# Kernel optimization log

Hardware: AMD Instinct MI355X
Metric: run time of the kernel (lower is better)

The kernel has to match this reference:

```python
import jax, jax.numpy as jnp
import numpy as np

NUM_HEADS = 12

def setup_inputs() -> dict:
    key = jax.random.key(0)
    ks = jax.random.split(key, 6)
    B, N, C, P = 16, 785, 768, 48
    return {
        "x": jax.random.normal(ks[0], (B, N, C), jnp.float32),
        "qkv_w": jax.random.normal(ks[1], (3 * C, C), jnp.float32) * 0.02,
        "pos_emb": jax.random.normal(ks[2], (N, N, P), jnp.float32) * 0.02,
        "pos_proj_w": jax.random.normal(ks[3], (NUM_HEADS, P), jnp.float32) * 0.02,
        "proj_w": jax.random.normal(ks[4], (C, C), jnp.float32) * 0.02,
        "proj_b": jnp.zeros((C,), jnp.float32),
    }

def reference(x, qkv_w, pos_emb, pos_proj_w, proj_w, proj_b):
    B, N, C = x.shape
    H = NUM_HEADS
    hd = C // H
    scale = hd ** -0.5
    # qkv projection: [B,N,3C] -> q,k,v each [B,H,N,hd]
    qkv = (x @ qkv_w.T).reshape(B, N, 3, H, hd)
    qkv = jnp.transpose(qkv, (2, 0, 3, 1, 4))
    q, k, v = qkv[0], qkv[1], qkv[2]
    # learned relative-position bias: [H,N,N]
    pos_score = jnp.einsum('nmp,hp->hnm', pos_emb, pos_proj_w)
    # attention scores: scale applied AFTER adding bias (matches original)
    attn = (jnp.einsum('bhnd,bhmd->bhnm', q, k) + pos_score[None]) * scale
    attn = jax.nn.softmax(attn, axis=-1)
    out = jnp.einsum('bhnm,bhmd->bhnd', attn, v)
    out = jnp.transpose(out, (0, 2, 1, 3)).reshape(B, N, C)
    return out @ proj_w.T + proj_b
```

## Files before the change

kernel.cpp:

```cpp
#include <hip/hip_runtime.h>
#include <hip/hip_fp16.h>

#define B_ 16
#define N_ 785
#define NP 800
#define C_ 768
#define H_ 12
#define HD_ 64
#define P_ 48
#define M_ (B_*N_)
#define MP_ (B_*NP)
#define POSW 832
#define VTW  832
#define SLOG2E 0.1803368801111244f

#define OFF_Q   0
#define OFF_K   9646080
#define OFF_VT  19292160
#define OFF_POS 29515776
#define OFF_XF  37353216
#define OFF_AO  OFF_XF
#define OFF_WQ  47085312
#define OFF_WP  48854784

struct __align__(16) Half8 { __half h[8]; };
typedef _Float16 half8_t __attribute__((ext_vector_type(8)));
typedef _Float16 half4_t __attribute__((ext_vector_type(4)));
typedef float f32x4 __attribute__((ext_vector_type(4)));

__device__ __forceinline__ void gl16(const void* g, void* l) {
    __builtin_amdgcn_global_load_lds(
        (const __attribute__((address_space(1))) void*)g,
        (__attribute__((address_space(3))) void*)l, 16, 0, 0);
}

__device__ __forceinline__ int xcd_swz(int o, int nwg) {
    const int q = nwg >> 3, r = nwg & 7;
    const int xcd = o & 7, idx = o >> 3;
    const int base = xcd < r ? xcd * (q + 1) : r * (q + 1) + (xcd - r) * q;
    return base + idx;
}

#define NX4 2411520
#define NQ4 442368
#define NP4 147456
#define NTOT4 (NX4+NQ4+NP4)

__global__ __launch_bounds__(256) void convert_f16(
    const float* __restrict__ x, const float* __restrict__ wq,
    const float* __restrict__ wp, _Float16* __restrict__ xo,
    _Float16* __restrict__ wqo, _Float16* __restrict__ wpo)
{
    int i = blockIdx.x * 256 + threadIdx.x;
    const float4* s; _Float16* d; int o;
    if (i < NX4)            { s = (const float4*)x;  d = xo;  o = i; }
    else if (i < NX4 + NQ4) { s = (const float4*)wq; d = wqo; o = i - NX4; }
    else                    { s = (const float4*)wp; d = wpo; o = i - NX4 - NQ4; }
    float4 v = s[o];
    half4_t h = { (_Float16)v.x, (_Float16)v.y, (_Float16)v.z, (_Float16)v.w };
    *(half4_t*)&d[o * 4] = h;
}

#define QKV_NWG (18 * 100)

__global__ __launch_bounds__(256) void qkv_gemm_mfma(
    const _Float16* __restrict__ A, const _Float16* __restrict__ Bw,
    _Float16* __restrict__ qh, _Float16* __restrict__ kh, _Float16* __restrict__ vth)
{
    __shared__ _Float16 Asl[2][128 * 64];
    __shared__ _Float16 Bsl[2][128 * 64];

    const int t  = threadIdx.x;
    const int w  = t >> 6;
    const int l  = t & 63;
    const int lr = l & 15;
    const int lg = l >> 4;
    const int wm = (w >> 1) * 64;
    const int wn = (w & 1) * 64;

    const int g   = xcd_swz(blockIdx.x, QKV_NWG);
    const int nt  = g % 18;
    const int n0  = nt * 128;
    const int mp0 = (g / 18) * 128;
    const int tsel  = nt / 6;
    const bool isV  = (tsel == 2);
    const int nbase = n0 - tsel * 768;

    const int row0 = t >> 2, row1 = 64 + (t >> 2);
    const int within = (t & 3) * 8;
    const int mpa0 = mp0 + row0, mpa1 = mp0 + row1;
    const int xra0 = (mpa0 / NP) * N_ + min(mpa0 % NP, N_ - 1);
    const int xra1 = (mpa1 / NP) * N_ + min(mpa1 % NP, N_ - 1);
    const _Float16* Ag0 = A  + (size_t)xra0 * 768 + within;
    const _Float16* Ag1 = A  + (size_t)xra1 * 768 + within;
    const _Float16* Bg0 = Bw + (size_t)(n0 + row0) * 768 + within;
    const _Float16* Bg1 = Bw + (size_t)(n0 + row1) * 768 + within;
    const int d0 = t * 8, d1 = (t + 256) * 8, d2 = (t + 512) * 8, d3 = (t + 768) * 8;

    f32x4 acc[4][4];
    #pragma unroll
    for (int i = 0; i < 4; ++i)
        #pragma unroll
        for (int j = 0; j < 4; ++j) acc[i][j] = (f32x4){0.f, 0.f, 0.f, 0.f};

    gl16(Ag0, &Asl[0][d0]); gl16(Ag1, &Asl[0][d1]);
    gl16(Ag0 + 32, &Asl[0][d2]); gl16(Ag1 + 32, &Asl[0][d3]);
    gl16(Bg0, &Bsl[0][d0]); gl16(Bg1, &Bsl[0][d1]);
    gl16(Bg0 + 32, &Bsl[0][d2]); gl16(Bg1 + 32, &Bsl[0][d3]);
    __syncthreads();

    for (int it = 0; it < 12; ++it) {
        const int cur = it & 1;
        if (it < 11) {
            const int kn = (it + 1) * 64;
            gl16(Ag0 + kn, &Asl[cur ^ 1][d0]); gl16(Ag1 + kn, &Asl[cur ^ 1][d1]);
            gl16(Ag0 + kn + 32, &Asl[cur ^ 1][d2]); gl16(Ag1 + kn + 32, &Asl[cur ^ 1][d3]);
            gl16(Bg0 + kn, &Bsl[cur ^ 1][d0]); gl16(Bg1 + kn, &Bsl[cur ^ 1][d1]);
            gl16(Bg0 + kn + 32, &Bsl[cur ^ 1][d2]); gl16(Bg1 + kn + 32, &Bsl[cur ^ 1][d3]);
        }
        #pragma unroll
        for (int kk = 0; kk < 2; ++kk) {
            const int kb = kk * 4096;
            half8_t af[4], bf[4];
            #pragma unroll
            for (int i = 0; i < 4; ++i)
                af[i] = *(const half8_t*)&Asl[cur][kb + (wm + i * 16 + lr) * 32 + lg * 8];
            #pragma unroll
            for (int j = 0; j < 4; ++j)
                bf[j] = *(const half8_t*)&Bsl[cur][kb + (wn + j * 16 + lr) * 32 + lg * 8];
            __builtin_amdgcn_s_setprio(1);
            if (!isV) {
                #pragma unroll
                for (int i = 0; i < 4; ++i)
                    #pragma unroll
                    for (int j = 0; j < 4; ++j)
                        acc[i][j] = __builtin_amdgcn_mfma_f32_16x16x32_f16(bf[j], af[i], acc[i][j], 0, 0, 0);
            } else {
                #pragma unroll
                for (int i = 0; i < 4; ++i)
                    #pragma unroll
                    for (int j = 0; j < 4; ++j)
                        acc[i][j] = __builtin_amdgcn_mfma_f32_16x16x32_f16(af[i], bf[j], acc[i][j], 0, 0, 0);
            }
            __builtin_amdgcn_s_setprio(0);
        }
        __syncthreads();
    }

    if (!isV) {
        _Float16* dstb = (tsel == 0) ? qh : kh;
        const float sc  = (tsel == 0) ? SLOG2E : 1.0f;
        #pragma unroll
        for (int i = 0; i < 4; ++i) {
            const int mp = mp0 + wm + i * 16 + lr;
            const int bb = mp / NP;
            const int nn = mp - bb * NP;
            if (nn >= N_) continue;
            #pragma unroll
            for (int j = 0; j < 4; ++j) {
                const int nq = nbase + wn + j * 16 + lg * 4;
                const int hh = nq >> 6, dd = nq & 63;
                half4_t hv = { (_Float16)(acc[i][j][0] * sc), (_Float16)(acc[i][j][1] * sc),
                               (_Float16)(acc[i][j][2] * sc), (_Float16)(acc[i][j][3] * sc) };
                *(half4_t*)(dstb + ((size_t)(bb * H_ + hh) * N_ + nn) * HD_ + dd) = hv;
            }
        }
    } else {
        #pragma unroll
        for (int i = 0; i < 4; ++i) {
            const int mq  = mp0 + wm + i * 16 + lg * 4;
            const int bb  = mq / NP;
            const int nn0 = mq - bb * NP;
            if (nn0 >= N_) continue;
            const bool full = (nn0 + 3) < N_;
            #pragma unroll
            for (int j = 0; j < 4; ++j) {
                const int n  = nbase + wn + j * 16 + lr;
                const int hh = n >> 6, dd = n & 63;
                _Float16* vb = vth + ((size_t)(bb * H_ + hh) * HD_ + dd) * VTW;
                if (full) {
                    half4_t hv = { (_Float16)acc[i][j][0], (_Float16)acc[i][j][1],
                                   (_Float16)acc[i][j][2], (_Float16)acc[i][j][3] };
                    *(half4_t*)(vb + nn0) = hv;
                } else {
                    #pragma unroll
                    for (int r = 0; r < 4; ++r)
                        if (nn0 + r < N_) vb[nn0 + r] = (_Float16)acc[i][j][r];
                }
            }
        }
    }
}

__global__ __launch_bounds__(256) void pos_kernel(
    const float* __restrict__ pe, const float* __restrict__ pw,
    __half* __restrict__ posh)
{
    __shared__ float W[H_][P_];
    const int t = threadIdx.x;
    for (int i = t; i < H_ * P_; i += 256) W[i / P_][i % P_] = pw[i];
    __syncthreads();
    int nm = blockIdx.x * 256 + t;
    if (nm >= N_ * N_) return;
    float e[48];
    const float4* src = (const float4*)(pe + (size_t)nm * 48);
    #pragma unroll
    for (int i = 0; i < 12; ++i) {
        float4 v = src[i];
        e[4*i] = v.x; e[4*i+1] = v.y; e[4*i+2] = v.z; e[4*i+3] = v.w;
    }
    int n = nm / N_, m = nm - n * N_;
    #pragma unroll
    for (int hh = 0; hh < H_; ++hh) {
        float s = 0.f;
        #pragma unroll
        for (int p = 0; p < 48; ++p) s = fmaf(e[p], W[hh][p], s);
        posh[((size_t)hh * N_ + n) * POSW + m] = __float2half(s * SLOG2E);
    }
}

#define NQT 13
#define ATT_NWG (192 * NQT)

__global__ __launch_bounds__(256) void attn_mfma(
    const _Float16* __restrict__ qh, const _Float16* __restrict__ kh,
    const _Float16* __restrict__ vt, const _Float16* __restrict__ posh,
    _Float16* __restrict__ aoh)
{
    __shared__ _Float16 Kl[2][64][72];
    __shared__ _Float16 Vl[2][64][72];

    const int t  = threadIdx.x;
    const int l  = t & 63;
    const int w  = t >> 6;
    const int lr = l & 15;
    const int lg = l >> 4;

    const int g2   = xcd_swz(blockIdx.x, ATT_NWG);
    const int qt   = g2 % NQT;
    const int rest = g2 / NQT;
    const int b    = rest & 15;
    const int h    = rest >> 4;
    const int bh   = b * H_ + h;
    const int n0   = qt * 64;

    const int qrow = n0 + w * 16 + lr;
    const int qrc  = qrow < N_ ? qrow : N_ - 1;
    const _Float16* qbase = qh + ((size_t)bh * N_ + qrc) * HD_;
    const half8_t qf0 = *(const half8_t*)(qbase + lg * 8);
    const half8_t qf1 = *(const half8_t*)(qbase + 32 + lg * 8);

    f32x4 O0 = {0.f,0.f,0.f,0.f}, O1 = O0, O2 = O0, O3 = O0;
    f32x4 lacc = {0.f,0.f,0.f,0.f};
    float m_run = 0.f;
    bool  virgin = true;

    const half8_t vones = { (_Float16)1.f, (_Float16)1.f, (_Float16)1.f, (_Float16)1.f,
                            (_Float16)1.f, (_Float16)1.f, (_Float16)1.f, (_Float16)1.f };

    const int srow = t >> 2;
    const int scol = (t & 3) * 16;
    const int vbase = (scol & 32) + ((scol & 16) >> 2);
    const _Float16* kRow = kh + ((size_t)bh * N_) * HD_ + scol;
    const _Float16* vRow = vt + ((size_t)bh * HD_ + srow) * VTW + scol;
    const _Float16* bFrag = posh + ((size_t)h * N_ + qrc) * POSW + lg * 4;

    half8_t rk0, rk1, rv0, rv1;
    half4_t rbc[4], rbn[4];
    {
        const int gm = srow < N_ ? srow : N_ - 1;
        const half8_t* ks = (const half8_t*)(kRow + (size_t)gm * HD_);
        rk0 = ks[0]; rk1 = ks[1];
        const half8_t* vs = (const half8_t*)vRow;
        rv0 = vs[0]; rv1 = vs[1];
        #pragma unroll
        for (int ms = 0; ms < 4; ++ms)
            rbc[ms] = *(const half4_t*)(bFrag + ms * 16);
    }
    *(half8_t*)&Kl[0][srow][scol]     = rk0;
    *(half8_t*)&Kl[0][srow][scol + 8] = rk1;
    {
        _Float16* vd = &Vl[0][srow][vbase];
        *(half4_t*)(vd +  0) = __builtin_shufflevector(rv0, rv0, 0, 1, 2, 3);
        *(half4_t*)(vd +  8) = __builtin_shufflevector(rv0, rv0, 4, 5, 6, 7);
        *(half4_t*)(vd + 16) = __builtin_shufflevector(rv1, rv1, 0, 1, 2, 3);
        *(half4_t*)(vd + 24) = __builtin_shufflevector(rv1, rv1, 4, 5, 6, 7);
    }

    for (int c = 0; c < 13; ++c) {
        const int cur = c & 1;
        __syncthreads();

        if (c < 12) {
            const int m0n = (c + 1) * 64;
            const int gm  = (m0n + srow) < N_ ? (m0n + srow) : N_ - 1;
            const half8_t* ks = (const half8_t*)(kRow + (size_t)gm * HD_);
            rk0 = ks[0]; rk1 = ks[1];
            const half8_t* vs = (const half8_t*)(vRow + m0n);
            rv0 = vs[0]; rv1 = vs[1];
            #pragma unroll
            for (int ms = 0; ms < 4; ++ms)
                rbn[ms] = *(const half4_t*)(bFrag + m0n + ms * 16);
        }

        f32x4 s[4];
        __builtin_amdgcn_s_setprio(1);
        #pragma unroll
        for (int ms = 0; ms < 4; ++ms) {
            f32x4 acc = { (float)rbc[ms][0], (float)rbc[ms][1],
                          (float)rbc[ms][2], (float)rbc[ms][3] };
            half8_t k0 = *(const half8_t*)&Kl[cur][ms * 16 + lr][lg * 8];
            half8_t k1 = *(const half8_t*)&Kl[cur][ms * 16 + lr][32 + lg * 8];
            acc = __builtin_amdgcn_mfma_f32_16x16x32_f16(k0, qf0, acc, 0, 0, 0);
            acc = __builtin_amdgcn_mfma_f32_16x16x32_f16(k1, qf1, acc, 0, 0, 0);
            s[ms] = acc;
        }
        __builtin_amdgcn_s_setprio(0);

        if (c == 12) {
            #pragma unroll
            for (int ms = 0; ms < 4; ++ms)
                #pragma unroll
                for (int r = 0; r < 4; ++r)
                    if (ms * 16 + lg * 4 + r >= 17) s[ms][r] = -1e30f;
        }

        float x0 = fmaxf(fmaxf(s[0][0], s[0][1]), s[0][2]);
        float x1 = fmaxf(fmaxf(s[0][3], s[1][0]), s[1][1]);
        float x2 = fmaxf(fmaxf(s[1][2], s[1][3]), s[2][0]);
        float x3 = fmaxf(fmaxf(s[2][1], s[2][2]), s[2][3]);
        float x4 = fmaxf(fmaxf(s[3][0], s[3][1]), s[3][2]);
        float mq = fmaxf(fmaxf(fmaxf(x0, x1), x2),
                         fmaxf(fmaxf(x3, x4), s[3][3]));

        if (__any(mq > m_run + 8.f)) {
            float v = fmaxf(mq, __shfl_xor(mq, 16));
            v = fmaxf(v, __shfl_xor(v, 32));
            const float mn    = fmaxf(m_run, v);
            const float alpha = exp2f(m_run - mn);
            m_run = mn;
            virgin = false;
            const float a0 = __shfl(alpha, lg * 4 + 0);
            const float a1 = __shfl(alpha, lg * 4 + 1);
            const float a2 = __shfl(alpha, lg * 4 + 2);
            const float a3 = __shfl(alpha, lg * 4 + 3);
            O0[0]*=a0; O0[1]*=a1; O0[2]*=a2; O0[3]*=a3;
            O1[0]*=a0; O1[1]*=a1; O1[2]*=a2; O1[3]*=a3;
            O2[0]*=a0; O2[1]*=a1; O2[2]*=a2; O2[3]*=a3;
            O3[0]*=a0; O3[1]*=a1; O3[2]*=a2; O3[3]*=a3;
            lacc[0]*=a0; lacc[1]*=a1; lacc[2]*=a2; lacc[3]*=a3;
        }

        float p[4][4];
        if (virgin) {
            #pragma unroll
            for (int ms = 0; ms < 4; ++ms)
                #pragma unroll
                for (int r = 0; r < 4; ++r)
                    p[ms][r] = exp2f(s[ms][r]);
        } else {
            #pragma unroll
            for (int ms = 0; ms < 4; ++ms)
                #pragma unroll
                for (int r = 0; r < 4; ++r)
                    p[ms][r] = exp2f(s[ms][r] - m_run);
        }

        half8_t pa0 = { (_Float16)p[0][0], (_Float16)p[0][1], (_Float16)p[0][2], (_Float16)p[0][3],
                        (_Float16)p[1][0], (_Float16)p[1][1], (_Float16)p[1][2], (_Float16)p[1][3] };
        half8_t pa1 = { (_Float16)p[2][0], (_Float16)p[2][1], (_Float16)p[2][2], (_Float16)p[2][3],
                        (_Float16)p[3][0], (_Float16)p[3][1], (_Float16)p[3][2], (_Float16)p[3][3] };

        if (c < 12) {
            const int nxt = cur ^ 1;
            *(half8_t*)&Kl[nxt][srow][scol]     = rk0;
            *(half8_t*)&Kl[nxt][srow][scol + 8] = rk1;
            _Float16* vd = &Vl[nxt][srow][vbase];
            *(half4_t*)(vd +  0) = __builtin_shufflevector(rv0, rv0, 0, 1, 2, 3);
            *(half4_t*)(vd +  8) = __builtin_shufflevector(rv0, rv0, 4, 5, 6, 7);
            *(half4_t*)(vd + 16) = __builtin_shufflevector(rv1, rv1, 0, 1, 2, 3);
            *(half4_t*)(vd + 24) = __builtin_shufflevector(rv1, rv1, 4, 5, 6, 7);
            #pragma unroll
            for (int ms = 0; ms < 4; ++ms) rbc[ms] = rbn[ms];
        }

        __builtin_amdgcn_s_setprio(1);
        lacc = __builtin_amdgcn_mfma_f32_16x16x32_f16(pa0, vones, lacc, 0, 0, 0);
        lacc = __builtin_amdgcn_mfma_f32_16x16x32_f16(pa1, vones, lacc, 0, 0, 0);
        #pragma unroll
        for (int ds = 0; ds < 4; ++ds) {
            const _Float16* vr = &Vl[cur][ds * 16 + lr][0];
            half8_t vf0 = *(const half8_t*)&vr[lg * 8];
            half8_t vf1 = *(const half8_t*)&vr[32 + lg * 8];
            f32x4& Od = (ds == 0 ? O0 : ds == 1 ? O1 : ds == 2 ? O2 : O3);
            Od = __builtin_amdgcn_mfma_f32_16x16x32_f16(pa0, vf0, Od, 0, 0, 0);
            Od = __builtin_amdgcn_mfma_f32_16x16x32_f16(pa1, vf1, Od, 0, 0, 0);
        }
        __builtin_amdgcn_s_setprio(0);
    }

    const int bb = bh / H_;
    #pragma unroll
    for (int r = 0; r < 4; ++r) {
        const int n = n0 + w * 16 + lg * 4 + r;
        if (n >= N_) continue;
        const float inv = 1.f / lacc[r];
        _Float16* dst = aoh + ((size_t)(bb * N_ + n)) * C_ + h * HD_;
        dst[0 * 16 + lr] = (_Float16)(O0[r] * inv);
        dst[1 * 16 + lr] = (_Float16)(O1[r] * inv);
        dst[2 * 16 + lr] = (_Float16)(O2[r] * inv);
        dst[3 * 16 + lr] = (_Float16)(O3[r] * inv);
    }
}

#define PROJ_NWG (6 * 99)

__global__ __launch_bounds__(256) void proj_gemm_mfma(
    const _Float16* __restrict__ A, const _Float16* __restrict__ Bw,
    const float* __restrict__ bias, float* __restrict__ out)
{
    __shared__ _Float16 Asl[2][128 * 64];
    __shared__ _Float16 Bsl[2][128 * 64];

    const int t  = threadIdx.x;
    const int w  = t >> 6;
    const int l  = t & 63;
    const int lr = l & 15;
    const int lg = l >> 4;
    const int wm = (w >> 1) * 64;
    const int wn = (w & 1) * 64;

    const int g  = xcd_swz(blockIdx.x, PROJ_NWG);
    const int n0 = (g % 6) * 128;
    const int m0 = (g / 6) * 128;

    const int row0 = t >> 2, row1 = 64 + (t >> 2);
    const int within = (t & 3) * 8;
    const int ma0 = min(m0 + row0, M_ - 1);
    const int ma1 = min(m0 + row1, M_ - 1);
    const _Float16* Ag0 = A  + (size_t)ma0 * 768 + within;
    const _Float16* Ag1 = A  + (size_t)ma1 * 768 + within;
    const _Float16* Bg0 = Bw + (size_t)(n0 + row0) * 768 + within;
    const _Float16* Bg1 = Bw + (size_t)(n0 + row1) * 768 + within;
    const int d0 = t * 8, d1 = (t + 256) * 8, d2 = (t + 512) * 8, d3 = (t + 768) * 8;

    f32x4 acc[4][4];
    #pragma unroll
    for (int i = 0; i < 4; ++i)
        #pragma unroll
        for (int j = 0; j < 4; ++j) acc[i][j] = (f32x4){0.f, 0.f, 0.f, 0.f};

    gl16(Ag0, &Asl[0][d0]); gl16(Ag1, &Asl[0][d1]);
    gl16(Ag0 + 32, &Asl[0][d2]); gl16(Ag1 + 32, &Asl[0][d3]);
    gl16(Bg0, &Bsl[0][d0]); gl16(Bg1, &Bsl[0][d1]);
    gl16(Bg0 + 32, &Bsl[0][d2]); gl16(Bg1 + 32, &Bsl[0][d3]);
    __syncthreads();

    for (int it = 0; it < 12; ++it) {
        const int cur = it & 1;
        if (it < 11) {
            const int kn = (it + 1) * 64;
            gl16(Ag0 + kn, &Asl[cur ^ 1][d0]); gl16(Ag1 + kn, &Asl[cur ^ 1][d1]);
            gl16(Ag0 + kn + 32, &Asl[cur ^ 1][d2]); gl16(Ag1 + kn + 32, &Asl[cur ^ 1][d3]);
            gl16(Bg0 + kn, &Bsl[cur ^ 1][d0]); gl16(Bg1 + kn, &Bsl[cur ^ 1][d1]);
            gl16(Bg0 + kn + 32, &Bsl[cur ^ 1][d2]); gl16(Bg1 + kn + 32, &Bsl[cur ^ 1][d3]);
        }
        #pragma unroll
        for (int kk = 0; kk < 2; ++kk) {
            const int kb = kk * 4096;
            half8_t af[4], bf[4];
            #pragma unroll
            for (int i = 0; i < 4; ++i)
                af[i] = *(const half8_t*)&Asl[cur][kb + (wm + i * 16 + lr) * 32 + lg * 8];
            #pragma unroll
            for (int j = 0; j < 4; ++j)
                bf[j] = *(const half8_t*)&Bsl[cur][kb + (wn + j * 16 + lr) * 32 + lg * 8];
            __builtin_amdgcn_s_setprio(1);
            #pragma unroll
            for (int i = 0; i < 4; ++i)
                #pragma unroll
                for (int j = 0; j < 4; ++j)
                    acc[i][j] = __builtin_amdgcn_mfma_f32_16x16x32_f16(bf[j], af[i], acc[i][j], 0, 0, 0);
            __builtin_amdgcn_s_setprio(0);
        }
        __syncthreads();
    }

    float4 bj4[4];
    #pragma unroll
    for (int j = 0; j < 4; ++j)
        bj4[j] = *(const float4*)&bias[n0 + wn + j * 16 + lg * 4];
    #pragma unroll
    for (int i = 0; i < 4; ++i) {
        const int m = m0 + wm + i * 16 + lr;
        if (m >= M_) continue;
        #pragma unroll
        for (int j = 0; j < 4; ++j) {
            const int nq = n0 + wn + j * 16 + lg * 4;
            float4 o = { acc[i][j][0] + bj4[j].x, acc[i][j][1] + bj4[j].y,
                         acc[i][j][2] + bj4[j].z, acc[i][j][3] + bj4[j].w };
            *(float4*)&out[(size_t)m * 768 + nq] = o;
        }
    }
}

extern "C" void kernel_launch(void* const* d_in, const int* in_sizes, int n_in,
                              void* d_out, int out_size, void* d_ws, size_t ws_size,
                              hipStream_t stream)
{
    const float* x     = (const float*)d_in[0];
    const float* qkv_w = (const float*)d_in[1];
    const float* pe    = (const float*)d_in[2];
    const float* pw    = (const float*)d_in[3];
    const float* pjw   = (const float*)d_in[4];
    const float* pjb   = (const float*)d_in[5];
    float* out = (float*)d_out;

    _Float16* wsh  = (_Float16*)d_ws;
    _Float16* qh   = wsh + OFF_Q;
    _Float16* kh   = wsh + OFF_K;
    _Float16* vth  = wsh + OFF_VT;
    _Float16* posh = wsh + OFF_POS;
    _Float16* xf   = wsh + OFF_XF;
    _Float16* aoh  = wsh + OFF_AO;
    _Float16* wqf  = wsh + OFF_WQ;
    _Float16* wpf  = wsh + OFF_WP;

    convert_f16<<<dim3(NTOT4 / 256), 256, 0, stream>>>(x, qkv_w, pjw, xf, wqf, wpf);
    qkv_gemm_mfma<<<dim3(QKV_NWG), 256, 0, stream>>>(xf, wqf, qh, kh, vth);
    pos_kernel<<<dim3((N_ * N_ + 255) / 256), 256, 0, stream>>>(pe, pw, (__half*)posh);
    attn_mfma<<<dim3(ATT_NWG), 256, 0, stream>>>(qh, kh, vth, posh, aoh);
    proj_gemm_mfma<<<dim3(PROJ_NWG), 256, 0, stream>>>(aoh, wpf, pjb, out);
}
```

Measured before the change: 253.0 us.

## Fuse QKV GEMM and positional-bias kernel into one interleaved launch

Merges the QKV projection GEMM and the memory-bound positional-score kernel into a single launch. Workgroup groups are split proportionally between the two tasks so compute-bound GEMM tiles and bandwidth-bound pos tiles run concurrently on the GPU. This also removes one kernel launch and the tail gap between the two. In exchange, the pos blocks now carry the GEMM's 64KB shared-memory allocation, which may lower occupancy for that part, and the XCD swizzle mapping changes.

```diff
diff --git a/kernel.cpp b/kernel.cpp
--- a/kernel.cpp
+++ b/kernel.cpp
@@ -61,161 +61,172 @@
     *(half4_t*)&d[o * 4] = h;
 }
 
-#define QKV_NWG (18 * 100)
-
-__global__ __launch_bounds__(256) void qkv_gemm_mfma(
+#define QKV_NWG 1800
+#define QKV_G   225
+#define POS_NWG 2408
+#define TOT_G   526
+#define FUSED_NWG (TOT_G * 8)
+
+__global__ __launch_bounds__(256) void qkv_pos_fused(
     const _Float16* __restrict__ A, const _Float16* __restrict__ Bw,
-    _Float16* __restrict__ qh, _Float16* __restrict__ kh, _Float16* __restrict__ vth)
+    _Float16* __restrict__ qh, _Float16* __restrict__ kh, _Float16* __restrict__ vth,
+    const float* __restrict__ pe, const float* __restrict__ pw,
+    _Float16* __restrict__ posh)
 {
-    __shared__ _Float16 Asl[2][128 * 64];
-    __shared__ _Float16 Bsl[2][128 * 64];
-
-    const int t  = threadIdx.x;
-    const int w  = t >> 6;
-    const int l  = t & 63;
-    const int lr = l & 15;
-    const int lg = l >> 4;
-    const int wm = (w >> 1) * 64;
-    const int wn = (w & 1) * 64;
-
-    const int g   = xcd_swz(blockIdx.x, QKV_NWG);
-    const int nt  = g % 18;
-    const int n0  = nt * 128;
-    const int mp0 = (g / 18) * 128;
-    const int tsel  = nt / 6;
-    const bool isV  = (tsel == 2);
-    const int nbase = n0 - tsel * 768;
-
-    const int row0 = t >> 2, row1 = 64 + (t >> 2);
-    const int within = (t & 3) * 8;
-    const int mpa0 = mp0 + row0, mpa1 = mp0 + row1;
-    const int xra0 = (mpa0 / NP) * N_ + min(mpa0 % NP, N_ - 1);
-    const int xra1 = (mpa1 / NP) * N_ + min(mpa1 % NP, N_ - 1);
-    const _Float16* Ag0 = A  + (size_t)xra0 * 768 + within;
-    const _Float16* Ag1 = A  + (size_t)xra1 * 768 + within;
-    const _Float16* Bg0 = Bw + (size_t)(n0 + row0) * 768 + within;
-    const _Float16* Bg1 = Bw + (size_t)(n0 + row1) * 768 + within;
-    const int d0 = t * 8, d1 = (t + 256) * 8, d2 = (t + 512) * 8, d3 = (t + 768) * 8;
-
-    f32x4 acc[4][4];
-    #pragma unroll
-    for (int i = 0; i < 4; ++i)
-        #pragma unroll
-        for (int j = 0; j < 4; ++j) acc[i][j] = (f32x4){0.f, 0.f, 0.f, 0.f};
-
-    gl16(Ag0, &Asl[0][d0]); gl16(Ag1, &Asl[0][d1]);
-    gl16(Ag0 + 32, &Asl[0][d2]); gl16(Ag1 + 32, &Asl[0][d3]);
-    gl16(Bg0, &Bsl[0][d0]); gl16(Bg1, &Bsl[0][d1]);
-    gl16(Bg0 + 32, &Bsl[0][d2]); gl16(Bg1 + 32, &Bsl[0][d3]);
-    __syncthreads();
-
-    for (int it = 0; it < 12; ++it) {
-        const int cur = it & 1;
-        if (it < 11) {
-            const int kn = (it + 1) * 64;
-            gl16(Ag0 + kn, &Asl[cur ^ 1][d0]); gl16(Ag1 + kn, &Asl[cur ^ 1][d1]);
-            gl16(Ag0 + kn + 32, &Asl[cur ^ 1][d2]); gl16(Ag1 + kn + 32, &Asl[cur ^ 1][d3]);
-            gl16(Bg0 + kn, &Bsl[cur ^ 1][d0]); gl16(Bg1 + kn, &Bsl[cur ^ 1][d1]);
-            gl16(Bg0 + kn + 32, &Bsl[cur ^ 1][d2]); gl16(Bg1 + kn + 32, &Bsl[cur ^ 1][d3]);
-        }
-        #pragma unroll
-        for (int kk = 0; kk < 2; ++kk) {
-            const int kb = kk * 4096;
-            half8_t af[4], bf[4];
-            #pragma unroll
-            for (int i = 0; i < 4; ++i)
-                af[i] = *(const half8_t*)&Asl[cur][kb + (wm + i * 16 + lr) * 32 + lg * 8];
-            #pragma unroll
-            for (int j = 0; j < 4; ++j)
-                bf[j] = *(const half8_t*)&Bsl[cur][kb + (wn + j * 16 + lr) * 32 + lg * 8];
-            __builtin_amdgcn_s_setprio(1);
-            if (!isV) {
+    __shared__ _Float16 smem[4 * 128 * 64];
+
+    const int t   = threadIdx.x;
+    const int gid = blockIdx.x;
+    const int G   = gid >> 3, sub = gid & 7;
+    const int aG  = (G * QKV_G) / TOT_G;
+    const int bG  = ((G + 1) * QKV_G) / TOT_G;
+
+    if (bG > aG) {
+        _Float16 (*Asl)[128 * 64] = (_Float16 (*)[128 * 64])(smem);
+        _Float16 (*Bsl)[128 * 64] = (_Float16 (*)[128 * 64])(smem + 2 * 128 * 64);
+
+        const int qid = aG * 8 + sub;
+        const int w  = t >> 6;
+        const int l  = t & 63;
+        const int lr = l & 15;
+        const int lg = l >> 4;
+        const int wm = (w >> 1) * 64;
+        const int wn = (w & 1) * 64;
+
+        const int g   = xcd_swz(qid, QKV_NWG);
+        const int nt  = g % 18;
+        const int n0  = nt * 128;
+        const int mp0 = (g / 18) * 128;
+        const int tsel  = nt / 6;
+        const bool isV  = (tsel == 2);
+        const int nbase = n0 - tsel * 768;
+
+        const int row0 = t >> 2, row1 = 64 + (t >> 2);
+        const int within = (t & 3) * 8;
+        const int mpa0 = mp0 + row0, mpa1 = mp0 + row1;
+        const int xra0 = (mpa0 / NP) * N_ + min(mpa0 % NP, N_ - 1);
+        const int xra1 = (mpa1 / NP) * N_ + min(mpa1 % NP, N_ - 1);
+        const _Float16* Ag0 = A  + (size_t)xra0 * 768 + within;
+        const _Float16* Ag1 = A  + (size_t)xra1 * 768 + within;
+        const _Float16* Bg0 = Bw + (size_t)(n0 + row0) * 768 + within;
+        const _Float16* Bg1 = Bw + (size_t)(n0 + row1) * 768 + within;
+        const int d0 = t * 8, d1 = (t + 256) * 8, d2 = (t + 512) * 8, d3 = (t + 768) * 8;
+
+        f32x4 acc[4][4];
+        #pragma unroll
+        for (int i = 0; i < 4; ++i)
+            #pragma unroll
+            for (int j = 0; j < 4; ++j) acc[i][j] = (f32x4){0.f, 0.f, 0.f, 0.f};
+
+        gl16(Ag0, &Asl[0][d0]); gl16(Ag1, &Asl[0][d1]);
+        gl16(Ag0 + 32, &Asl[0][d2]); gl16(Ag1 + 32, &Asl[0][d3]);
+        gl16(Bg0, &Bsl[0][d0]); gl16(Bg1, &Bsl[0][d1]);
+        gl16(Bg0 + 32, &Bsl[0][d2]); gl16(Bg1 + 32, &Bsl[0][d3]);
+        __syncthreads();
+
+        for (int it = 0; it < 12; ++it) {
+            const int cur = it & 1;
+            if (it < 11) {
+                const int kn = (it + 1) * 64;
+                gl16(Ag0 + kn, &Asl[cur ^ 1][d0]); gl16(Ag1 + kn, &Asl[cur ^ 1][d1]);
+                gl16(Ag0 + kn + 32, &Asl[cur ^ 1][d2]); gl16(Ag1 + kn + 32, &Asl[cur ^ 1][d3]);
+                gl16(Bg0 + kn, &Bsl[cur ^ 1][d0]); gl16(Bg1 + kn, &Bsl[cur ^ 1][d1]);
+                gl16(Bg0 + kn + 32, &Bsl[cur ^ 1][d2]); gl16(Bg1 + kn + 32, &Bsl[cur ^ 1][d3]);
+            }
+            #pragma unroll
+            for (int kk = 0; kk < 2; ++kk) {
+                const int kb = kk * 4096;
+                half8_t af[4], bf[4];
                 #pragma unroll
                 for (int i = 0; i < 4; ++i)
+                    af[i] = *(const half8_t*)&Asl[cur][kb + (wm + i * 16 + lr) * 32 + lg * 8];
+                #pragma unroll
+                for (int j = 0; j < 4; ++j)
+                    bf[j] = *(const half8_t*)&Bsl[cur][kb + (wn + j * 16 + lr) * 32 + lg * 8];
+                __builtin_amdgcn_s_setprio(1);
+                if (!isV) {
                     #pragma unroll
-                    for (int j = 0; j < 4; ++j)
-                        acc[i][j] = __builtin_amdgcn_mfma_f32_16x16x32_f16(bf[j], af[i], acc[i][j], 0, 0, 0);
-            } else {
-                #pragma unroll
-                for (int i = 0; i < 4; ++i)
-                    #pragma unroll
-                    for (int j = 0; j < 4; ++j)
-                        acc[i][j] = __builtin_amdgcn_mfma_f32_16x16x32_f16(af[i], bf[j], acc[i][j], 0, 0, 0);
-            }
-            __builtin_amdgcn_s_setprio(0);
-        }
-        __syncthreads();
-    }
-
-    if (!isV) {
-        _Float16* dstb = (tsel == 0) ? qh : kh;
-        const float sc  = (tsel == 0) ? SLOG2E : 1.0f;
-        #pragma unroll
-        for (int i = 0; i < 4; ++i) {
-            const int mp = mp0 + wm + i * 16 + lr;
-            const int bb = mp / NP;
-            const int nn = mp - bb * NP;
-            if (nn >= N_) continue;
-            #pragma unroll
-            for (int j = 0; j < 4; ++j) {
-                const int nq = nbase + wn + j * 16 + lg * 4;
-                const int hh = nq >> 6, dd = nq & 63;
-                half4_t hv = { (_Float16)(acc[i][j][0] * sc), (_Float16)(acc[i][j][1] * sc),
-                               (_Float16)(acc[i][j][2] * sc), (_Float16)(acc[i][j][3] * sc) };
-                *(half4_t*)(dstb + ((size_t)(bb * H_ + hh) * N_ + nn) * HD_ + dd) = hv;
-            }
-        }
-    } else {
-        #pragma unroll
-        for (int i = 0; i < 4; ++i) {
-            const int mq  = mp0 + wm + i * 16 + lg * 4;
-            const int bb  = mq / NP;
-            const int nn0 = mq - bb * NP;
-            if (nn0 >= N_) continue;
-            const bool full = (nn0 + 3) < N_;
-            #pragma unroll
-            for (int j = 0; j < 4; ++j) {
-                const int n  = nbase + wn + j * 16 + lr;
-                const int hh = n >> 6, dd = n & 63;
-                _Float16* vb = vth + ((size_t)(bb * H_ + hh) * HD_ + dd) * VTW;
-                if (full) {
-                    half4_t hv = { (_Float16)acc[i][j][0], (_Float16)acc[i][j][1],
-                                   (_Float16)acc[i][j][2], (_Float16)acc[i][j][3] };
-                    *(half4_t*)(vb + nn0) = hv;
+                    for (int i = 0; i < 4; ++i)
+                        #pragma unroll
+                        for (int j = 0; j < 4; ++j)
+                            acc[i][j] = __builtin_amdgcn_mfma_f32_16x16x32_f16(bf[j], af[i], acc[i][j], 0, 0, 0);
                 } else {
                     #pragma unroll
-                    for (int r = 0; r < 4; ++r)
-                        if (nn0 + r < N_) vb[nn0 + r] = (_Float16)acc[i][j][r];
+                    for (int i = 0; i < 4; ++i)
+                        #pragma unroll
+                        for (int j = 0; j < 4; ++j)
+                            acc[i][j] = __builtin_amdgcn_mfma_f32_16x16x32_f16(af[i], bf[j], acc[i][j], 0, 0, 0);
+                }
+                __builtin_amdgcn_s_setprio(0);
+            }
+            __syncthreads();
+        }
+
+        if (!isV) {
+            _Float16* dstb = (tsel == 0) ? qh : kh;
+            const float sc  = (tsel == 0) ? SLOG2E : 1.0f;
+            #pragma unroll
+            for (int i = 0; i < 4; ++i) {
+                const int mp = mp0 + wm + i * 16 + lr;
+                const int bb = mp / NP;
+                const int nn = mp - bb * NP;
+                if (nn >= N_) continue;
+                #pragma unroll
+                for (int j = 0; j < 4; ++j) {
+                    const int nq = nbase + wn + j * 16 + lg * 4;
+                    const int hh = nq >> 6, dd = nq & 63;
+                    half4_t hv = { (_Float16)(acc[i][j][0] * sc), (_Float16)(acc[i][j][1] * sc),
+                                   (_Float16)(acc[i][j][2] * sc), (_Float16)(acc[i][j][3] * sc) };
+                    *(half4_t*)(dstb + ((size_t)(bb * H_ + hh) * N_ + nn) * HD_ + dd) = hv;
                 }
             }
-        }
-    }
-}
-
-__global__ __launch_bounds__(256) void pos_kernel(
-    const float* __restrict__ pe, const float* __restrict__ pw,
-    __half* __restrict__ posh)
-{
-    __shared__ float W[H_][P_];
-    const int t = threadIdx.x;
-    for (int i = t; i < H_ * P_; i += 256) W[i / P_][i % P_] = pw[i];
-    __syncthreads();
-    int nm = blockIdx.x * 256 + t;
-    if (nm >= N_ * N_) return;
-    float e[48];
-    const float4* src = (const float4*)(pe + (size_t)nm * 48);
-    #pragma unroll
-    for (int i = 0; i < 12; ++i) {
-        float4 v = src[i];
-        e[4*i] = v.x; e[4*i+1] = v.y; e[4*i+2] = v.z; e[4*i+3] = v.w;
-    }
-    int n = nm / N_, m = nm - n * N_;
-    #pragma unroll
-    for (int hh = 0; hh < H_; ++hh) {
-        float s = 0.f;
-        #pragma unroll
-        for (int p = 0; p < 48; ++p) s = fmaf(e[p], W[hh][p], s);
-        posh[((size_t)hh * N_ + n) * POSW + m] = __float2half(s * SLOG2E);
+        } else {
+            #pragma unroll
+            for (int i = 0; i < 4; ++i) {
+                const int mq  = mp0 + wm + i * 16 + lg * 4;
+                const int bb  = mq / NP;
+                const int nn0 = mq - bb * NP;
+                if (nn0 >= N_) continue;
+                const bool full = (nn0 + 3) < N_;
+                #pragma unroll
+                for (int j = 0; j < 4; ++j) {
+                    const int n  = nbase + wn + j * 16 + lr;
+                    const int hh = n >> 6, dd = n & 63;
+                    _Float16* vb = vth + ((size_t)(bb * H_ + hh) * HD_ + dd) * VTW;
+                    if (full) {
+                        half4_t hv = { (_Float16)acc[i][j][0], (_Float16)acc[i][j][1],
+                                       (_Float16)acc[i][j][2], (_Float16)acc[i][j][3] };
+                        *(half4_t*)(vb + nn0) = hv;
+                    } else {
+                        #pragma unroll
+                        for (int r = 0; r < 4; ++r)
+                            if (nn0 + r < N_) vb[nn0 + r] = (_Float16)acc[i][j][r];
+                    }
+                }
+            }
+        }
+    } else {
+        float* W = (float*)smem;
+        const int pid = (G - aG) * 8 + sub;
+        for (int i = t; i < H_ * P_; i += 256) W[i] = pw[i];
+        __syncthreads();
+        const int nm = pid * 256 + t;
+        if (nm >= N_ * N_) return;
+        float e[48];
+        const float4* src = (const float4*)(pe + (size_t)nm * 48);
+        #pragma unroll
+        for (int i = 0; i < 12; ++i) {
+            float4 v = src[i];
+            e[4*i] = v.x; e[4*i+1] = v.y; e[4*i+2] = v.z; e[4*i+3] = v.w;
+        }
+        const int n = nm / N_, m = nm - n * N_;
+        #pragma unroll
+        for (int hh = 0; hh < H_; ++hh) {
+            float s = 0.f;
+            #pragma unroll
+            for (int p = 0; p < 48; ++p) s = fmaf(e[p], W[hh * P_ + p], s);
+            posh[((size_t)hh * N_ + n) * POSW + m] = (_Float16)(s * SLOG2E);
+        }
     }
 }
 
@@ -527,8 +538,8 @@
     _Float16* wpf  = wsh + OFF_WP;
 
     convert_f16<<<dim3(NTOT4 / 256), 256, 0, stream>>>(x, qkv_w, pjw, xf, wqf, wpf);
-    qkv_gemm_mfma<<<dim3(QKV_NWG), 256, 0, stream>>>(xf, wqf, qh, kh, vth);
-    pos_kernel<<<dim3((N_ * N_ + 255) / 256), 256, 0, stream>>>(pe, pw, (__half*)posh);
+    qkv_pos_fused<<<dim3(FUSED_NWG), 256, 0, stream>>>(
+        xf, wqf, qh, kh, vth, pe, pw, posh);
     attn_mfma<<<dim3(ATT_NWG), 256, 0, stream>>>(qh, kh, vth, posh, aoh);
     proj_gemm_mfma<<<dim3(PROJ_NWG), 256, 0, stream>>>(aoh, wpf, pjb, out);
 }
```

Result: slower. 275.3 us (+8.8%).
